# Kernel tuning notes

Hardware: AMD Instinct MI355X
Metric: run time of the kernel (lower is better)

## Reference

```python
import jax, jax.numpy as jnp
import numpy as np

D_MODEL = 512
NUM_HEADS = 8
D_HEAD = D_MODEL // NUM_HEADS
D_POS = D_MODEL // 4  # pos_encoding output dim
LN_EPS = 1e-5


def setup_inputs() -> dict:
    key = jax.random.key(0)
    ks = jax.random.split(key, 10)
    B, N = 2, 4096
    s = 1.0 / np.sqrt(D_MODEL)
    return {
        "positions": jax.random.normal(ks[0], (B, N, 3), jnp.float32),
        "features": jax.random.normal(ks[1], (B, N, D_MODEL), jnp.float32),
        "k_neighbors": 16,
        # learned params; torch Linear y = x @ W.T, we store W as [in, out]
        "Wq": jax.random.normal(ks[2], (D_MODEL, D_MODEL), jnp.float32) * s,
        "Wk": jax.random.normal(ks[3], (D_MODEL, D_MODEL), jnp.float32) * s,
        "Wv": jax.random.normal(ks[4], (D_MODEL, D_MODEL), jnp.float32) * s,
        "Wo": jax.random.normal(ks[5], (D_MODEL, D_MODEL), jnp.float32) * s,
        "bo": jnp.zeros((D_MODEL,), jnp.float32),
        "Wpos": jax.random.normal(ks[6], (3, D_POS), jnp.float32) * 0.5,
        "bpos": jnp.zeros((D_POS,), jnp.float32),
        "temperature": jnp.full((1,), np.sqrt(D_HEAD), jnp.float32),
        "ln_gamma": jnp.ones((D_MODEL,), jnp.float32),
        "ln_beta": jnp.zeros((D_MODEL,), jnp.float32),
    }


def _layer_norm(x, gamma, beta):
    mu = jnp.mean(x, axis=-1, keepdims=True)
    var = jnp.mean(jnp.square(x - mu), axis=-1, keepdims=True)
    return (x - mu) * jax.lax.rsqrt(var + LN_EPS) * gamma + beta


def reference(positions, features, k_neighbors, Wq, Wk, Wv, Wo, bo, Wpos, bpos,
              temperature, ln_gamma, ln_beta):
    B, N, Dm = features.shape
    H, Dh = NUM_HEADS, D_HEAD

    # ---- kNN via full pairwise squared distances (as in source) ----
    diff = positions[:, :, None, :] - positions[:, None, :, :]      # [B,N,N,3]
    sq_dists = jnp.sum(diff * diff, axis=-1)                        # [B,N,N]
    _, idx = jax.lax.top_k(-sq_dists, k_neighbors + 1)              # smallest dists
    idx = idx[:, :, 1:k_neighbors + 1]                              # drop self -> [B,N,k]

    nb_pos = jax.vmap(lambda p, i: p[i])(positions, idx)            # [B,N,k,3]
    rel_pos = positions[:, :, None, :] - nb_pos                     # [B,N,k,3]

    # ---- projections ----
    def split_heads(x):
        return x.reshape(B, N, H, Dh).transpose(0, 2, 1, 3)         # [B,H,N,Dh]
    q = split_heads(features @ Wq)
    k = split_heads(features @ Wk)
    v = split_heads(features @ Wv)

    # ---- gather neighbor K/V: per-batch fancy index over N axis ----
    kg = jax.vmap(lambda t, i: t[:, i])(k, idx)                     # [B,H,N,k,Dh]
    vg = jax.vmap(lambda t, i: t[:, i])(v, idx)                     # [B,H,N,k,Dh]

    # ---- fused positional encoding (repeat x4 then slice to d_head) ----
    pe = rel_pos @ Wpos + bpos                                      # [B,N,k,D_POS]
    pe = jnp.tile(pe, (1, 1, 1, 4))[..., :Dh]                       # [B,N,k,Dh]
    kg = kg + pe[:, None]                                           # broadcast heads

    # ---- local softmax attention over k neighbors ----
    scores = jnp.einsum('bhnd,bhnkd->bhnk', q, kg) / temperature[0]
    w = jax.nn.softmax(scores, axis=-1)                             # [B,H,N,k]
    att = jnp.einsum('bhnk,bhnkd->bhnd', w, vg)                     # [B,H,N,Dh]

    out = att.transpose(0, 2, 1, 3).reshape(B, N, Dm) @ Wo + bo
    return _layer_norm(out + features, ln_gamma, ln_beta)
```

## Files before the change

kernel.cpp:

```cpp
#include <hip/hip_runtime.h>
#include <cstdint>

#define D_MODEL 512
#define NUM_HEADS 8
#define D_HEAD 64
#define KNB 16
#define NBUCK 2048
#define LN_EPS 1e-5f
#define FINF 3.4e38f

typedef __bf16 bf16x8v __attribute__((ext_vector_type(8)));
typedef float f32x4v __attribute__((ext_vector_type(4)));
typedef int i32x4 __attribute__((ext_vector_type(4)));
typedef const __attribute__((address_space(1))) unsigned int* gptr_t;
typedef __attribute__((address_space(3))) unsigned int* lptr_t;

__device__ __forceinline__ float wave_reduce_sum(float v) {
  #pragma unroll
  for (int off = 32; off > 0; off >>= 1) v += __shfl_xor(v, off, 64);
  return v;
}

__device__ __forceinline__ unsigned short f2bf(float x) {
  unsigned int u = __float_as_uint(x);
  u = (u + 0x7fffu + ((u >> 16) & 1u)) >> 16;
  return (unsigned short)u;
}
__device__ __forceinline__ float bf2f(unsigned short h) {
  return __uint_as_float(((unsigned int)h) << 16);
}

__device__ __forceinline__ unsigned spread3(unsigned x) {
  x &= 0x3FFu;
  x = (x | (x << 16)) & 0x030000FFu;
  x = (x | (x << 8))  & 0x0300F00Fu;
  x = (x | (x << 4))  & 0x030C30C3u;
  x = (x | (x << 2))  & 0x09249249u;
  return x;
}
__device__ __forceinline__ unsigned quant10(float v) {
  int q = (int)((v + 6.f) * (1023.f / 12.f));
  q = q < 0 ? 0 : (q > 1023 ? 1023 : q);
  return (unsigned)q;
}

__device__ __forceinline__ void bitonic64(float& d, int& j, int lane) {
  #pragma unroll
  for (int k = 2; k <= 64; k <<= 1) {
    #pragma unroll
    for (int s = k >> 1; s > 0; s >>= 1) {
      const float od = __shfl_xor(d, s, 64);
      const int   oj = __shfl_xor(j, s, 64);
      const bool up = ((lane & k) == 0);
      const bool lower = ((lane & s) == 0);
      const bool oless = (od < d) || (od == d && oj < j);
      if ((lower == up) ? oless : !oless) { d = od; j = oj; }
    }
  }
}

__global__ void zero_hist_kernel(int* __restrict__ hist, int n) {
  const int t = blockIdx.x * blockDim.x + threadIdx.x;
  if (t < n) hist[t] = 0;
}

__global__ void bucket_kernel(const float* __restrict__ pos,
                              float4* __restrict__ posf4,
                              int* __restrict__ hist,
                              int* __restrict__ bucketid, int total) {
  const int t = blockIdx.x * blockDim.x + threadIdx.x;
  if (t >= total) return;
  const float4 p = make_float4(pos[t * 3], pos[t * 3 + 1], pos[t * 3 + 2], 0.f);
  posf4[t] = p;
  const unsigned code = (spread3(quant10(p.z)) << 2) |
                        (spread3(quant10(p.y)) << 1) | spread3(quant10(p.x));
  const int bk = code >> 19;
  const int b = t >> 12;
  bucketid[t] = bk;
  atomicAdd(&hist[b * NBUCK + bk], 1);
}

__global__ __launch_bounds__(1024) void scan_kernel(const int* __restrict__ hist,
                                                    int* __restrict__ off) {
  __shared__ int lsum[16];
  const int b = blockIdx.x;
  const int tid = threadIdx.x;
  const int lane = tid & 63, wv = tid >> 6;
  const int h0 = hist[b * NBUCK + 2 * tid];
  const int h1 = hist[b * NBUCK + 2 * tid + 1];
  int v = h0 + h1;
  #pragma unroll
  for (int d = 1; d < 64; d <<= 1) {
    const int u = __shfl_up(v, d, 64);
    if (lane >= d) v += u;
  }
  if (lane == 63) lsum[wv] = v;
  __syncthreads();
  if (wv == 0) {
    int s = (lane < 16) ? lsum[lane] : 0;
    #pragma unroll
    for (int d = 1; d < 16; d <<= 1) {
      const int u = __shfl_up(s, d, 64);
      if (lane >= d) s += u;
    }
    if (lane < 16) lsum[lane] = s;
  }
  __syncthreads();
  const int base = (wv > 0) ? lsum[wv - 1] : 0;
  const int excl = v + base - (h0 + h1);
  off[b * NBUCK + 2 * tid] = excl;
  off[b * NBUCK + 2 * tid + 1] = excl + h0;
}

__global__ void scatter_kernel(const float4* __restrict__ posf4,
                               const int* __restrict__ bucketid,
                               int* __restrict__ off,
                               int* __restrict__ perm,
                               float4* __restrict__ posf4s, int total) {
  const int t = blockIdx.x * blockDim.x + threadIdx.x;
  if (t >= total) return;
  const int b = t >> 12;
  const int i = t & 4095;
  const int slot = atomicAdd(&off[b * NBUCK + bucketid[t]], 1);
  perm[b * 4096 + slot] = i;
  posf4s[b * 4096 + slot] = posf4[t];
}

__global__ __launch_bounds__(512, 4) void knn_kernel(const float4* __restrict__ posf4s,
                                                     int* __restrict__ idx_out,
                                                     int N) {
  __shared__ float4 pts[4096];
  __shared__ float scrD[16 * 64];
  __shared__ int   scrJ[16 * 64];

  const int tid = threadIdx.x;
  const int lane = tid & 63;
  const int wid = tid >> 6;
  const int qs0 = blockIdx.x * 16 + wid * 2;
  const int base = qs0 & ~4095;
  const int n0 = qs0 & 4095;
  const int n1 = n0 + 1;
  const float4* pb = posf4s + base;

  #pragma unroll
  for (int i = 0; i < 8; ++i) {
    const int c = wid * 8 + i;
    __builtin_amdgcn_global_load_lds((gptr_t)(pb + c * 64 + lane),
                                     (lptr_t)&pts[c * 64], 16, 0, 0);
  }
  __syncthreads();

  const float4 qp0 = pts[n0];
  const float4 qp1 = pts[n1];

  float lmin0 = FINF, lmin1 = FINF;
  #pragma unroll 8
  for (int it = 0; it < 64; ++it) {
    const int j = (it << 6) + lane;
    const float4 p = pts[j];
    float dx = qp0.x - p.x, dy = qp0.y - p.y, dz = qp0.z - p.z;
    float d0 = dx * dx + dy * dy + dz * dz;
    dx = qp1.x - p.x; dy = qp1.y - p.y; dz = qp1.z - p.z;
    float d1 = dx * dx + dy * dy + dz * dz;
    if (j == n0) d0 = FINF;
    if (j == n1) d1 = FINF;
    lmin0 = fminf(lmin0, d0);
    lmin1 = fminf(lmin1, d1);
  }

  float a0 = lmin0, a1 = lmin1;
  #pragma unroll
  for (int k = 2; k <= 64; k <<= 1) {
    #pragma unroll
    for (int s = k >> 1; s > 0; s >>= 1) {
      const bool keepmin = (((lane & k) == 0) == ((lane & s) == 0));
      const float b0 = __shfl_xor(a0, s, 64);
      const float b1 = __shfl_xor(a1, s, 64);
      a0 = keepmin ? fminf(a0, b0) : fmaxf(a0, b0);
      a1 = keepmin ? fminf(a1, b1) : fmaxf(a1, b1);
    }
  }
  float tau0 = __shfl(a0, 15, 64);
  float tau1 = __shfl(a1, 15, 64);

  const unsigned long long lt = (1ull << lane) - 1ull;
  const int wq0 = wid * 2, wq1 = wid * 2 + 1;
  int cnt0 = 0, cnt1 = 0;
  #pragma unroll 4
  for (int it = 0; it < 64; ++it) {
    const int j = (it << 6) + lane;
    const float4 p = pts[j];
    float dx = qp0.x - p.x, dy = qp0.y - p.y, dz = qp0.z - p.z;
    float d0 = dx * dx + dy * dy + dz * dz;
    dx = qp1.x - p.x; dy = qp1.y - p.y; dz = qp1.z - p.z;
    float d1 = dx * dx + dy * dy + dz * dz;
    if (j == n0) d0 = FINF;
    if (j == n1) d1 = FINF;
    const bool p0 = (d0 <= tau0);
    const bool p1 = (d1 <= tau1);
    const unsigned long long m0 = __ballot(p0);
    const unsigned long long m1 = __ballot(p1);
    if (p0) {
      const int s0 = cnt0 + __popcll(m0 & lt);
      if (s0 < 64) { scrD[wq0 * 64 + s0] = d0; scrJ[wq0 * 64 + s0] = j; }
    }
    if (p1) {
      const int s1 = cnt1 + __popcll(m1 & lt);
      if (s1 < 64) { scrD[wq1 * 64 + s1] = d1; scrJ[wq1 * 64 + s1] = j; }
    }
    cnt0 += (int)__popcll(m0);
    cnt1 += (int)__popcll(m1);
  }

  for (int q = 0; q < 2; ++q) {
    const int wq = wid * 2 + q;
    int cnt = q ? cnt1 : cnt0;
    float tau = q ? tau1 : tau0;
    const float4 qp = q ? qp1 : qp0;
    const int n = q ? n1 : n0;
    const int qs = qs0 + q;

    int m = cnt < 64 ? cnt : 64;
    float d = (lane < m) ? scrD[wq * 64 + lane] : FINF;
    int  jj = (lane < m) ? scrJ[wq * 64 + lane] : 0x40000000 + lane;
    bitonic64(d, jj, lane);

    while (cnt > 64) {
      const float ntau = __shfl(d, 15, 64);
      if (!(ntau < tau)) break;
      tau = ntau;
      cnt = 0;
      #pragma unroll 4
      for (int it = 0; it < 64; ++it) {
        const int j = (it << 6) + lane;
        const float4 p = pts[j];
        const float ddx = qp.x - p.x, ddy = qp.y - p.y, ddz = qp.z - p.z;
        float dd = ddx * ddx + ddy * ddy + ddz * ddz;
        if (j == n) dd = FINF;
        const bool pr = (dd <= tau);
        const unsigned long long mm = __ballot(pr);
        if (pr) {
          const int sl = cnt + __popcll(mm & lt);
          if (sl < 64) { scrD[wq * 64 + sl] = dd; scrJ[wq * 64 + sl] = j; }
        }
        cnt += (int)__popcll(mm);
      }
      m = cnt < 64 ? cnt : 64;
      d = (lane < m) ? scrD[wq * 64 + lane] : FINF;
      jj = (lane < m) ? scrJ[wq * 64 + lane] : 0x40000000 + lane;
      bitonic64(d, jj, lane);
    }

    if (lane < KNB) idx_out[(size_t)qs * KNB + lane] = jj;
  }
}

__global__ __launch_bounds__(256) void conv_kernel(const float* __restrict__ src,
                                                   const int* __restrict__ perm,
                                                   unsigned short* __restrict__ dst,
                                                   const float* __restrict__ Wq,
                                                   const float* __restrict__ Wk,
                                                   const float* __restrict__ Wv,
                                                   const float* __restrict__ Wo,
                                                   unsigned short* __restrict__ BhQKV,
                                                   unsigned short* __restrict__ BlQKV,
                                                   unsigned short* __restrict__ BhO,
                                                   unsigned short* __restrict__ BlO) {
  const int b = blockIdx.x;
  if (b < 4096) {
    const int t = b * 256 + threadIdx.x;
    const int f = t * 4;
    const int row = f >> 9;
    const int col = f & 511;
    const int orig = (row & ~4095) + perm[row];
    const float4 v = *(const float4*)(src + (size_t)orig * 512 + col);
    ushort4 h, l;
    h.x = f2bf(v.x); l.x = f2bf(v.x - bf2f(h.x));
    h.y = f2bf(v.y); l.y = f2bf(v.y - bf2f(h.y));
    h.z = f2bf(v.z); l.z = f2bf(v.z - bf2f(h.z));
    h.w = f2bf(v.w); l.w = f2bf(v.w - bf2f(h.w));
    *(ushort4*)(dst + (size_t)row * 1024 + col) = h;
    *(ushort4*)(dst + (size_t)row * 1024 + 512 + col) = l;
  } else {
    const int bb = b - 4096;
    const int wsel = bb >> 10;
    const int i = ((bb & 1023) << 8) + threadIdx.x;
    const int n = i >> 9;
    const int k = i & 511;
    const float* wsrc = wsel == 0 ? Wq : wsel == 1 ? Wk : wsel == 2 ? Wv : Wo;
    unsigned short* dh = wsel < 3 ? BhQKV + (size_t)(wsel * 512 + n) * 512
                                  : BhO + (size_t)n * 512;
    unsigned short* dl = wsel < 3 ? BlQKV + (size_t)(wsel * 512 + n) * 512
                                  : BlO + (size_t)n * 512;
    const float w = wsrc[(size_t)k * 512 + n];
    const unsigned short h = f2bf(w);
    dh[k] = h;
    dl[k] = f2bf(w - bf2f(h));
  }
}

__global__ __launch_bounds__(256, 2) void gemm_split_kernel(
    const unsigned short* __restrict__ A,
    const unsigned short* __restrict__ Bh,
    const unsigned short* __restrict__ Bl,
    float* __restrict__ C0, float* __restrict__ C1, float* __restrict__ C2,
    int nbn) {
  __shared__ unsigned short AsH[8192];
  __shared__ unsigned short AsL[8192];
  __shared__ unsigned short Bs[8192];

  const int tid = threadIdx.x;
  const int wid = tid >> 6;
  const int lane = tid & 63;
  const int lm = lane & 15;
  const int kq = lane >> 4;
  const int wr = wid >> 1;
  const int wc = wid & 1;
  const int bid = blockIdx.x;
  const int xcd = bid & 7;
  const int i = bid >> 3;
  const int bm = xcd * 8 + i / nbn;
  const int bn = i % nbn;
  const int rowA0 = bm * 128;
  const int rowB0 = bn * 128;

  f32x4v acc[4][4];
  #pragma unroll
  for (int mi = 0; mi < 4; ++mi)
    #pragma unroll
    for (int ni = 0; ni < 4; ++ni) {
      f32x4v z = {0.f, 0.f, 0.f, 0.f};
      acc[mi][ni] = z;
    }

  auto stage64 = [&](unsigned short* dst, const unsigned short* gsrc,
                     int gstride, int grow0, int gk0) {
    #pragma unroll
    for (int i2 = 0; i2 < 4; ++i2) {
      const int c = wid * 256 + i2 * 64 + lane;
      const int row = c >> 3;
      const int gq = (c & 7) ^ (row & 7);
      const unsigned short* ga =
          gsrc + (size_t)(grow0 + row) * gstride + gk0 + gq * 8;
      __builtin_amdgcn_global_load_lds((gptr_t)ga,
          (lptr_t)(dst + (size_t)(wid * 256 + i2 * 64) * 8), 16, 0, 0);
    }
  };
  auto rd64 = [&](const unsigned short* src, int row, int g) -> i32x4 {
    const int sl = row * 8 + (g ^ (row & 7));
    return *(const i32x4*)(src + (size_t)sl * 8);
  };

  stage64(AsH, A, 1024, rowA0, 0);
  stage64(AsL, A, 1024, rowA0, 512);
  stage64(Bs, Bh, 512, rowB0, 0);

  for (int k0 = 0; k0 < 512; k0 += 64) {
    __syncthreads();
    i32x4 ah[2][4], al[2][4], bh[2][4];
    #pragma unroll
    for (int kh = 0; kh < 2; ++kh) {
      const int g = kh * 4 + kq;
      #pragma unroll
      for (int mi = 0; mi < 4; ++mi) {
        ah[kh][mi] = rd64(AsH, wr * 64 + mi * 16 + lm, g);
        al[kh][mi] = rd64(AsL, wr * 64 + mi * 16 + lm, g);
      }
      #pragma unroll
      for (int ni = 0; ni < 4; ++ni)
        bh[kh][ni] = rd64(Bs, wc * 64 + ni * 16 + lm, g);
    }
    __syncthreads();

    if (k0 < 448) {
      stage64(AsH, A, 1024, rowA0, k0 + 64);
      stage64(AsL, A, 1024, rowA0, 512 + k0 + 64);
      stage64(Bs, Bh, 512, rowB0, k0 + 64);
    } else {
      stage64(Bs, Bl, 512, rowB0, 448);
    }

    #pragma unroll
    for (int kh = 0; kh < 2; ++kh)
      #pragma unroll
      for (int mi = 0; mi < 4; ++mi)
        #pragma unroll
        for (int ni = 0; ni < 4; ++ni) {
          acc[mi][ni] = __builtin_amdgcn_mfma_f32_16x16x32_bf16(
              __builtin_bit_cast(bf16x8v, ah[kh][mi]),
              __builtin_bit_cast(bf16x8v, bh[kh][ni]), acc[mi][ni], 0, 0, 0);
          acc[mi][ni] = __builtin_amdgcn_mfma_f32_16x16x32_bf16(
              __builtin_bit_cast(bf16x8v, al[kh][mi]),
              __builtin_bit_cast(bf16x8v, bh[kh][ni]), acc[mi][ni], 0, 0, 0);
        }
  }

  for (int k0 = 448; k0 >= 0; k0 -= 64) {
    __syncthreads();
    i32x4 ah[2][4], bl[2][4];
    #pragma unroll
    for (int kh = 0; kh < 2; ++kh) {
      const int g = kh * 4 + kq;
      #pragma unroll
      for (int mi = 0; mi < 4; ++mi)
        ah[kh][mi] = rd64(AsH, wr * 64 + mi * 16 + lm, g);
      #pragma unroll
      for (int ni = 0; ni < 4; ++ni)
        bl[kh][ni] = rd64(Bs, wc * 64 + ni * 16 + lm, g);
    }
    __syncthreads();

    if (k0 > 0) {
      stage64(AsH, A, 1024, rowA0, k0 - 64);
      stage64(Bs, Bl, 512, rowB0, k0 - 64);
    }

    #pragma unroll
    for (int kh = 0; kh < 2; ++kh)
      #pragma unroll
      for (int mi = 0; mi < 4; ++mi)
        #pragma unroll
        for (int ni = 0; ni < 4; ++ni)
          acc[mi][ni] = __builtin_amdgcn_mfma_f32_16x16x32_bf16(
              __builtin_bit_cast(bf16x8v, ah[kh][mi]),
              __builtin_bit_cast(bf16x8v, bl[kh][ni]), acc[mi][ni], 0, 0, 0);
  }

  const int sel = bn >> 2;
  float* __restrict__ Cb = sel == 0 ? C0 : sel == 1 ? C1 : C2;
  const int r0 = bm * 128 + wr * 64;
  const int c0 = ((bn & 3) << 7) + wc * 64;
  #pragma unroll
  for (int mi = 0; mi < 4; ++mi)
    #pragma unroll
    for (int ni = 0; ni < 4; ++ni) {
      float* Cp = Cb + (size_t)(r0 + mi * 16 + kq * 4) * 512 + c0 + ni * 16 + lm;
      #pragma unroll
      for (int r = 0; r < 4; ++r) Cp[(size_t)r * 512] = acc[mi][ni][r];
    }
}

__global__ __launch_bounds__(256) void attn_kernel(const float* __restrict__ Q,
                                                   const float* __restrict__ Kb,
                                                   const float* __restrict__ Vb,
                                                   const int* __restrict__ idx,
                                                   const float4* __restrict__ posf4s,
                                                   const float* __restrict__ Wpos,
                                                   const float* __restrict__ bpos,
                                                   const float* __restrict__ temperature,
                                                   unsigned short* __restrict__ Aout,
                                                   int nblocks) {
  int bid = blockIdx.x;
  bid = (bid & 7) * (nblocks >> 3) + (bid >> 3);
  const int qs = bid * 4 + (threadIdx.x >> 6);
  const int lane = threadIdx.x & 63;
  const int s = lane & 7;
  const int base = qs & ~4095;

  const float inv_t = 1.0f / temperature[0];

  float q[8];
  *(float4*)&q[0] = *(const float4*)(Q + (size_t)qs * D_MODEL + lane * 8);
  *(float4*)&q[4] = *(const float4*)(Q + (size_t)qs * D_MODEL + lane * 8 + 4);

  float wp[3][8], bp[8];
  #pragma unroll
  for (int c = 0; c < 3; ++c) {
    *(float4*)&wp[c][0] = *(const float4*)(Wpos + c * 128 + s * 8);
    *(float4*)&wp[c][4] = *(const float4*)(Wpos + c * 128 + s * 8 + 4);
  }
  *(float4*)&bp[0] = *(const float4*)(bpos + s * 8);
  *(float4*)&bp[4] = *(const float4*)(bpos + s * 8 + 4);
  float qw0 = 0.f, qw1 = 0.f, qw2 = 0.f, qb = 0.f;
  #pragma unroll
  for (int j = 0; j < 8; ++j) {
    qw0 += q[j] * wp[0][j];
    qw1 += q[j] * wp[1][j];
    qw2 += q[j] * wp[2][j];
    qb  += q[j] * bp[j];
  }
  #pragma unroll
  for (int off = 1; off < 8; off <<= 1) {
    qw0 += __shfl_xor(qw0, off, 64);
    qw1 += __shfl_xor(qw1, off, 64);
    qw2 += __shfl_xor(qw2, off, 64);
    qb  += __shfl_xor(qb, off, 64);
  }

  const float4 qp = posf4s[qs];
  const int* ip = idx + (size_t)qs * KNB;
  int nb[KNB];
  #pragma unroll
  for (int k = 0; k < KNB; ++k) nb[k] = base + ip[k];

  float pe[KNB];
  {
    float4 np[KNB];
    #pragma unroll
    for (int k = 0; k < KNB; ++k) np[k] = posf4s[nb[k]];
    #pragma unroll
    for (int k = 0; k < KNB; ++k)
      pe[k] = qw0 * (qp.x - np[k].x) + qw1 * (qp.y - np[k].y) +
              qw2 * (qp.z - np[k].z) + qb;
  }

  float sc[KNB];
  #pragma unroll
  for (int kb = 0; kb < KNB; kb += 8) {
    float kk[8][8];
    #pragma unroll
    for (int k = 0; k < 8; ++k) {
      const float* kr = Kb + (size_t)nb[kb + k] * D_MODEL + lane * 8;
      *(float4*)&kk[k][0] = *(const float4*)(kr);
      *(float4*)&kk[k][4] = *(const float4*)(kr + 4);
    }
    #pragma unroll
    for (int k = 0; k < 8; ++k) {
      float pdot = 0.f;
      #pragma unroll
      for (int j2 = 0; j2 < 8; ++j2) pdot += q[j2] * kk[k][j2];
      #pragma unroll
      for (int off = 1; off < 8; off <<= 1) pdot += __shfl_xor(pdot, off, 64);
      sc[kb + k] = (pdot + pe[kb + k]) * inv_t;
    }
  }

  float m = sc[0];
  #pragma unroll
  for (int k = 1; k < KNB; ++k) m = fmaxf(m, sc[k]);
  float ssum = 0.f;
  #pragma unroll
  for (int k = 0; k < KNB; ++k) { sc[k] = expf(sc[k] - m); ssum += sc[k]; }
  const float inv_s = 1.f / ssum;

  float acc[8];
  #pragma unroll
  for (int j = 0; j < 8; ++j) acc[j] = 0.f;
  #pragma unroll
  for (int kb = 0; kb < KNB; kb += 8) {
    float vv[8][8];
    #pragma unroll
    for (int k = 0; k < 8; ++k) {
      const float* vr = Vb + (size_t)nb[kb + k] * D_MODEL + lane * 8;
      *(float4*)&vv[k][0] = *(const float4*)(vr);
      *(float4*)&vv[k][4] = *(const float4*)(vr + 4);
    }
    #pragma unroll
    for (int k = 0; k < 8; ++k) {
      const float wk = sc[kb + k];
      #pragma unroll
      for (int j = 0; j < 8; ++j) acc[j] += wk * vv[k][j];
    }
  }

  ushort4 hi0, hi1, lo0, lo1;
  unsigned short* oh = Aout + (size_t)qs * 1024 + lane * 8;
  unsigned short* ol = oh + 512;
  float a0 = acc[0] * inv_s, a1 = acc[1] * inv_s, a2 = acc[2] * inv_s, a3 = acc[3] * inv_s;
  float a4 = acc[4] * inv_s, a5 = acc[5] * inv_s, a6 = acc[6] * inv_s, a7 = acc[7] * inv_s;
  hi0.x = f2bf(a0); lo0.x = f2bf(a0 - bf2f(hi0.x));
  hi0.y = f2bf(a1); lo0.y = f2bf(a1 - bf2f(hi0.y));
  hi0.z = f2bf(a2); lo0.z = f2bf(a2 - bf2f(hi0.z));
  hi0.w = f2bf(a3); lo0.w = f2bf(a3 - bf2f(hi0.w));
  hi1.x = f2bf(a4); lo1.x = f2bf(a4 - bf2f(hi1.x));
  hi1.y = f2bf(a5); lo1.y = f2bf(a5 - bf2f(hi1.y));
  hi1.z = f2bf(a6); lo1.z = f2bf(a6 - bf2f(hi1.z));
  hi1.w = f2bf(a7); lo1.w = f2bf(a7 - bf2f(hi1.w));
  *(ushort4*)(oh) = hi0;
  *(ushort4*)(oh + 4) = hi1;
  *(ushort4*)(ol) = lo0;
  *(ushort4*)(ol + 4) = lo1;
}

__global__ __launch_bounds__(256) void ln_kernel(const float* __restrict__ proj,
                                                 const float* __restrict__ feat,
                                                 const int* __restrict__ perm,
                                                 const float* __restrict__ bo,
                                                 const float* __restrict__ gamma,
                                                 const float* __restrict__ beta,
                                                 float* __restrict__ out) {
  const int row = blockIdx.x * 4 + (threadIdx.x >> 6);
  const int lane = threadIdx.x & 63;
  const int orig = (row & ~4095) + perm[row];
  const float* pr = proj + (size_t)row * D_MODEL;
  const float* fr = feat + (size_t)orig * D_MODEL;

  float x[8];
  #pragma unroll
  for (int u = 0; u < 2; ++u) {
    const int c = u * 256 + lane * 4;
    const float4 p = *(const float4*)(pr + c);
    const float4 f = *(const float4*)(fr + c);
    const float4 bb = *(const float4*)(bo + c);
    x[u * 4 + 0] = p.x + bb.x + f.x;
    x[u * 4 + 1] = p.y + bb.y + f.y;
    x[u * 4 + 2] = p.z + bb.z + f.z;
    x[u * 4 + 3] = p.w + bb.w + f.w;
  }
  float sum = 0.f, sumsq = 0.f;
  #pragma unroll
  for (int i = 0; i < 8; ++i) { sum += x[i]; sumsq += x[i] * x[i]; }
  sum = wave_reduce_sum(sum);
  sumsq = wave_reduce_sum(sumsq);
  const float mu = sum * (1.f / D_MODEL);
  const float var = sumsq * (1.f / D_MODEL) - mu * mu;
  const float rstd = rsqrtf(var + LN_EPS);

  #pragma unroll
  for (int u = 0; u < 2; ++u) {
    const int c = u * 256 + lane * 4;
    const float4 g = *(const float4*)(gamma + c);
    const float4 bt = *(const float4*)(beta + c);
    float4 o;
    o.x = (x[u * 4 + 0] - mu) * rstd * g.x + bt.x;
    o.y = (x[u * 4 + 1] - mu) * rstd * g.y + bt.y;
    o.z = (x[u * 4 + 2] - mu) * rstd * g.z + bt.z;
    o.w = (x[u * 4 + 3] - mu) * rstd * g.w + bt.w;
    *(float4*)(out + (size_t)orig * D_MODEL + c) = o;
  }
}

extern "C" void kernel_launch(void* const* d_in, const int* in_sizes, int n_in,
                              void* d_out, int out_size, void* d_ws, size_t ws_size,
                              hipStream_t stream) {
  const float* positions = (const float*)d_in[0];
  const float* features  = (const float*)d_in[1];
  const float* Wq   = (const float*)d_in[3];
  const float* Wk   = (const float*)d_in[4];
  const float* Wv   = (const float*)d_in[5];
  const float* Wo   = (const float*)d_in[6];
  const float* bo   = (const float*)d_in[7];
  const float* Wpos = (const float*)d_in[8];
  const float* bpos = (const float*)d_in[9];
  const float* temp = (const float*)d_in[10];
  const float* gamma = (const float*)d_in[11];
  const float* beta  = (const float*)d_in[12];

  const int B = 2, N = 4096;
  const int BN = B * N;

  char* w = (char*)d_ws;
  float4* posf4  = (float4*)w;             w += (size_t)BN * sizeof(float4);
  float4* posf4s = (float4*)w;             w += (size_t)BN * sizeof(float4);
  int*    idxb   = (int*)w;                w += (size_t)BN * KNB * sizeof(int);
  int*    permb  = (int*)w;                w += (size_t)BN * sizeof(int);
  int*    histb  = (int*)w;                w += (size_t)B * NBUCK * sizeof(int);
  int*    offb   = (int*)w;                w += (size_t)B * NBUCK * sizeof(int);
  int*    buckb  = (int*)w;                w += (size_t)BN * sizeof(int);
  unsigned short* Abuf = (unsigned short*)w; w += (size_t)BN * 1024 * 2;
  unsigned short* BhQKV = (unsigned short*)w; w += (size_t)1536 * 512 * 2;
  unsigned short* BlQKV = (unsigned short*)w; w += (size_t)1536 * 512 * 2;
  unsigned short* BhO = (unsigned short*)w;   w += (size_t)512 * 512 * 2;
  unsigned short* BlO = (unsigned short*)w;   w += (size_t)512 * 512 * 2;
  float* Qb   = (float*)w;                 w += (size_t)BN * D_MODEL * sizeof(float);
  float* Kbuf = (float*)w;                 w += (size_t)BN * D_MODEL * sizeof(float);
  float* Vbuf = (float*)d_out;
  float* projb = Kbuf;

  zero_hist_kernel<<<(B * NBUCK + 255) / 256, 256, 0, stream>>>(histb, B * NBUCK);
  bucket_kernel<<<(BN + 255) / 256, 256, 0, stream>>>(positions, posf4, histb,
                                                      buckb, BN);
  scan_kernel<<<B, 1024, 0, stream>>>(histb, offb);
  scatter_kernel<<<(BN + 255) / 256, 256, 0, stream>>>(posf4, buckb, offb,
                                                       permb, posf4s, BN);
  knn_kernel<<<BN / 16, 512, 0, stream>>>(posf4s, idxb, N);

  conv_kernel<<<8192, 256, 0, stream>>>(features, permb, Abuf,
                                        Wq, Wk, Wv, Wo,
                                        BhQKV, BlQKV, BhO, BlO);

  gemm_split_kernel<<<768, 256, 0, stream>>>(
      Abuf, BhQKV, BlQKV, Qb, Kbuf, Vbuf, 12);

  attn_kernel<<<BN / 4, 256, 0, stream>>>(Qb, Kbuf, Vbuf, idxb,
                                          posf4s, Wpos, bpos, temp, Abuf,
                                          BN / 4);

  gemm_split_kernel<<<256, 256, 0, stream>>>(
      Abuf, BhO, BlO, projb, projb, projb, 4);

  ln_kernel<<<BN / 4, 256, 0, stream>>>(projb, features, permb, bo, gamma, beta,
                                        (float*)d_out);
}
```

Measured before the change: 246.0 us.

## Split attention neighbors across two waves per query with LDS softmax merge

Each query's 16 neighbors are split between two waves of 8 each. Each wave computes a partial softmax (max, sum, weighted V accumulation), and the two halves are merged through shared memory with a flash-style rescale before the bf16 hi/lo output is written. The launch grid doubles to keep one query per wave pair. The aim is more parallelism and memory-level concurrency with fewer registers per wave on the gather-bound attention step. The cost is a __syncthreads, LDS traffic, and one wave of each pair sitting idle during the output write.

```diff
diff --git a/kernel.cpp b/kernel.cpp
--- a/kernel.cpp
+++ b/kernel.cpp
@@ -450,11 +450,18 @@
                                                    const float* __restrict__ temperature,
                                                    unsigned short* __restrict__ Aout,
                                                    int nblocks) {
+  __shared__ float mS[4][8], sS[4][8];
+  __shared__ float accHalf[2][512];
+
   int bid = blockIdx.x;
   bid = (bid & 7) * (nblocks >> 3) + (bid >> 3);
-  const int qs = bid * 4 + (threadIdx.x >> 6);
+  const int wid = threadIdx.x >> 6;
   const int lane = threadIdx.x & 63;
+  const int qi = wid >> 1;
+  const int hf = wid & 1;
+  const int qs = bid * 2 + qi;
   const int s = lane & 7;
+  const int grp = lane >> 3;
   const int base = qs & ~4095;
 
   const float inv_t = 1.0f / temperature[0];
@@ -488,29 +495,28 @@
   }
 
   const float4 qp = posf4s[qs];
-  const int* ip = idx + (size_t)qs * KNB;
-  int nb[KNB];
-  #pragma unroll
-  for (int k = 0; k < KNB; ++k) nb[k] = base + ip[k];
-
-  float pe[KNB];
+  const int* ip = idx + (size_t)qs * KNB + hf * 8;
+  int nb[8];
+  #pragma unroll
+  for (int k = 0; k < 8; ++k) nb[k] = base + ip[k];
+
+  float pe[8];
   {
-    float4 np[KNB];
-    #pragma unroll
-    for (int k = 0; k < KNB; ++k) np[k] = posf4s[nb[k]];
-    #pragma unroll
-    for (int k = 0; k < KNB; ++k)
+    float4 np[8];
+    #pragma unroll
+    for (int k = 0; k < 8; ++k) np[k] = posf4s[nb[k]];
+    #pragma unroll
+    for (int k = 0; k < 8; ++k)
       pe[k] = qw0 * (qp.x - np[k].x) + qw1 * (qp.y - np[k].y) +
               qw2 * (qp.z - np[k].z) + qb;
   }
 
-  float sc[KNB];
-  #pragma unroll
-  for (int kb = 0; kb < KNB; kb += 8) {
+  float sc[8];
+  {
     float kk[8][8];
     #pragma unroll
     for (int k = 0; k < 8; ++k) {
-      const float* kr = Kb + (size_t)nb[kb + k] * D_MODEL + lane * 8;
+      const float* kr = Kb + (size_t)nb[k] * D_MODEL + lane * 8;
       *(float4*)&kk[k][0] = *(const float4*)(kr);
       *(float4*)&kk[k][4] = *(const float4*)(kr + 4);
     }
@@ -521,55 +527,71 @@
       for (int j2 = 0; j2 < 8; ++j2) pdot += q[j2] * kk[k][j2];
       #pragma unroll
       for (int off = 1; off < 8; off <<= 1) pdot += __shfl_xor(pdot, off, 64);
-      sc[kb + k] = (pdot + pe[kb + k]) * inv_t;
+      sc[k] = (pdot + pe[k]) * inv_t;
     }
   }
 
   float m = sc[0];
   #pragma unroll
-  for (int k = 1; k < KNB; ++k) m = fmaxf(m, sc[k]);
+  for (int k = 1; k < 8; ++k) m = fmaxf(m, sc[k]);
   float ssum = 0.f;
   #pragma unroll
-  for (int k = 0; k < KNB; ++k) { sc[k] = expf(sc[k] - m); ssum += sc[k]; }
-  const float inv_s = 1.f / ssum;
+  for (int k = 0; k < 8; ++k) { sc[k] = expf(sc[k] - m); ssum += sc[k]; }
 
   float acc[8];
   #pragma unroll
   for (int j = 0; j < 8; ++j) acc[j] = 0.f;
-  #pragma unroll
-  for (int kb = 0; kb < KNB; kb += 8) {
+  {
     float vv[8][8];
     #pragma unroll
     for (int k = 0; k < 8; ++k) {
-      const float* vr = Vb + (size_t)nb[kb + k] * D_MODEL + lane * 8;
+      const float* vr = Vb + (size_t)nb[k] * D_MODEL + lane * 8;
       *(float4*)&vv[k][0] = *(const float4*)(vr);
       *(float4*)&vv[k][4] = *(const float4*)(vr + 4);
     }
     #pragma unroll
     for (int k = 0; k < 8; ++k) {
-      const float wk = sc[kb + k];
+      const float wk = sc[k];
       #pragma unroll
       for (int j = 0; j < 8; ++j) acc[j] += wk * vv[k][j];
     }
   }
 
-  ushort4 hi0, hi1, lo0, lo1;
-  unsigned short* oh = Aout + (size_t)qs * 1024 + lane * 8;
-  unsigned short* ol = oh + 512;
-  float a0 = acc[0] * inv_s, a1 = acc[1] * inv_s, a2 = acc[2] * inv_s, a3 = acc[3] * inv_s;
-  float a4 = acc[4] * inv_s, a5 = acc[5] * inv_s, a6 = acc[6] * inv_s, a7 = acc[7] * inv_s;
-  hi0.x = f2bf(a0); lo0.x = f2bf(a0 - bf2f(hi0.x));
-  hi0.y = f2bf(a1); lo0.y = f2bf(a1 - bf2f(hi0.y));
-  hi0.z = f2bf(a2); lo0.z = f2bf(a2 - bf2f(hi0.z));
-  hi0.w = f2bf(a3); lo0.w = f2bf(a3 - bf2f(hi0.w));
-  hi1.x = f2bf(a4); lo1.x = f2bf(a4 - bf2f(hi1.x));
-  hi1.y = f2bf(a5); lo1.y = f2bf(a5 - bf2f(hi1.y));
-  hi1.z = f2bf(a6); lo1.z = f2bf(a6 - bf2f(hi1.z));
-  hi1.w = f2bf(a7); lo1.w = f2bf(a7 - bf2f(hi1.w));
-  *(ushort4*)(oh) = hi0;
-  *(ushort4*)(oh + 4) = hi1;
-  *(ushort4*)(ol) = lo0;
-  *(ushort4*)(ol + 4) = lo1;
+  if ((lane & 7) == 0) { mS[wid][grp] = m; sS[wid][grp] = ssum; }
+  if (hf == 1) {
+    #pragma unroll
+    for (int j = 0; j < 8; ++j) accHalf[qi][j * 64 + lane] = acc[j];
+  }
+  __syncthreads();
+  if (hf == 0) {
+    const float mB = mS[wid + 1][grp];
+    const float sB = sS[wid + 1][grp];
+    const float M = fmaxf(m, mB);
+    const float wA = expf(m - M);
+    const float wB = expf(mB - M);
+    const float inv_s = 1.f / (ssum * wA + sB * wB);
+
+    float a[8];
+    #pragma unroll
+    for (int j = 0; j < 8; ++j)
+      a[j] = (acc[j] * wA + accHalf[qi][j * 64 + lane] * wB) * inv_s;
+
+    ushort4 hi0, hi1, lo0, lo1;
+    unsigned short* oh = Aout + (size_t)qs * 1024 + lane * 8;
+    unsigned short* ol = oh + 512;
+    hi0.x = f2bf(a[0]); lo0.x = f2bf(a[0] - bf2f(hi0.x));
+    hi0.y = f2bf(a[1]); lo0.y = f2bf(a[1] - bf2f(hi0.y));
+    hi0.z = f2bf(a[2]); lo0.z = f2bf(a[2] - bf2f(hi0.z));
+    hi0.w = f2bf(a[3]); lo0.w = f2bf(a[3] - bf2f(hi0.w));
+    hi1.x = f2bf(a[4]); lo1.x = f2bf(a[4] - bf2f(hi1.x));
+    hi1.y = f2bf(a[5]); lo1.y = f2bf(a[5] - bf2f(hi1.y));
+    hi1.z = f2bf(a[6]); lo1.z = f2bf(a[6] - bf2f(hi1.z));
+    hi1.w = f2bf(a[7]); lo1.w = f2bf(a[7] - bf2f(hi1.w));
+    *(ushort4*)(oh) = hi0;
+    *(ushort4*)(oh + 4) = hi1;
+    *(ushort4*)(ol) = lo0;
+    *(ushort4*)(ol + 4) = lo1;
+  }
 }
 
 __global__ __launch_bounds__(256) void ln_kernel(const float* __restrict__ proj,
@@ -672,9 +694,9 @@
   gemm_split_kernel<<<768, 256, 0, stream>>>(
       Abuf, BhQKV, BlQKV, Qb, Kbuf, Vbuf, 12);
 
-  attn_kernel<<<BN / 4, 256, 0, stream>>>(Qb, Kbuf, Vbuf, idxb,
+  attn_kernel<<<BN / 2, 256, 0, stream>>>(Qb, Kbuf, Vbuf, idxb,
                                           posf4s, Wpos, bpos, temp, Abuf,
-                                          BN / 4);
+                                          BN / 2);
 
   gemm_split_kernel<<<256, 256, 0, stream>>>(
       Abuf, BhO, BlO, projb, projb, projb, 4);
```

Measured after the change: 249.3 us. No clear change (+1.3%).
